# Performance work log

Measured on AMD Instinct MI355X. Metric: run time of the kernel, lower is better.

The kernel has to match this reference:

```python
import jax, jax.numpy as jnp
import numpy as np


def _grid_sample_3d(src, grid):
    """Trilinear grid_sample, align_corners=True, zero padding.
    src: [B,C,D,H,W], grid: [B,D,H,W,3] with last dim (x,y,z) ~ (W,H,D) in [-1,1].
    """
    B, C, D, H, W = src.shape
    gx, gy, gz = grid[..., 0], grid[..., 1], grid[..., 2]
    # unnormalize (align_corners=True): -1 -> 0, +1 -> dim-1
    ix = (gx + 1.0) * ((W - 1) / 2.0)
    iy = (gy + 1.0) * ((H - 1) / 2.0)
    iz = (gz + 1.0) * ((D - 1) / 2.0)
    ix0 = jnp.floor(ix); iy0 = jnp.floor(iy); iz0 = jnp.floor(iz)
    fx = ix - ix0; fy = iy - iy0; fz = iz - iz0  # fractional parts
    x0 = ix0.astype(jnp.int32); y0 = iy0.astype(jnp.int32); z0 = iz0.astype(jnp.int32)

    src_flat = src.reshape(B, C, D * H * W)
    out = jnp.zeros((B, C, D * H * W), dtype=src.dtype)
    for dz in (0, 1):
        for dy in (0, 1):
            for dx in (0, 1):
                xc = x0 + dx; yc = y0 + dy; zc = z0 + dz
                w = ((fx if dx else 1.0 - fx)
                     * (fy if dy else 1.0 - fy)
                     * (fz if dz else 1.0 - fz))
                valid = ((xc >= 0) & (xc < W) & (yc >= 0) & (yc < H)
                         & (zc >= 0) & (zc < D))
                xs = jnp.clip(xc, 0, W - 1)
                ys = jnp.clip(yc, 0, H - 1)
                zs = jnp.clip(zc, 0, D - 1)
                lin = ((zs * H + ys) * W + xs).reshape(B, -1)  # [B, DHW]
                vals = jax.vmap(lambda s, i: jnp.take(s, i, axis=1))(src_flat, lin)  # [B,C,DHW]
                out = out + (w * valid).reshape(B, 1, -1).astype(src.dtype) * vals
    return out.reshape(B, C, D, H, W)


def _affine_grid_3d(theta, D, H, W):
    """torch affine_grid (align_corners=True) for size [B,3,D,H,W]. Returns [B,D,H,W,3]."""
    xs = jnp.linspace(-1.0, 1.0, W, dtype=theta.dtype)
    ys = jnp.linspace(-1.0, 1.0, H, dtype=theta.dtype)
    zs = jnp.linspace(-1.0, 1.0, D, dtype=theta.dtype)
    bx = jnp.broadcast_to(xs[None, None, :], (D, H, W))
    by = jnp.broadcast_to(ys[None, :, None], (D, H, W))
    bz = jnp.broadcast_to(zs[:, None, None], (D, H, W))
    base = jnp.stack([bx, by, bz, jnp.ones((D, H, W), theta.dtype)], axis=-1)  # [D,H,W,4]
    return jnp.einsum('bij,dhwj->bdhwi', theta, base)


def setup_inputs() -> dict:
    key = jax.random.key(0)
    k1, k2 = jax.random.split(key)
    B, C, D, H, W = 2, 2, 160, 192, 224
    src = jax.random.normal(k1, (B, C, D, H, W), dtype=jnp.float32)
    eye = jnp.concatenate([jnp.eye(3, dtype=jnp.float32),
                           jnp.zeros((3, 1), jnp.float32)], axis=1)  # [3,4]
    mat = eye[None] + 0.05 * jax.random.normal(k2, (B, 3, 4), dtype=jnp.float32)
    return {"src": src, "mat": mat}


def reference(src, mat):
    B, C, D, H, W = src.shape
    norm = jnp.array([[1, 1, 1, D], [1, 1, 1, H], [1, 1, 1, W]], dtype=mat.dtype)
    theta = mat / norm[None]  # normalize translation column by spatial dims
    grid = _affine_grid_3d(theta, D, H, W)
    return _grid_sample_3d(src, grid)
```

## Files before the change

kernel.cpp:

```cpp
#include <hip/hip_runtime.h>

#define BB 2
#define CC 2
#define DD 160
#define HH 192
#define WW 224
#define DHW (DD * HH * WW)

typedef float f2v __attribute__((ext_vector_type(2)));

__device__ __forceinline__ f2v load2u(const float* p) {
    struct __attribute__((packed)) S { f2v v; };
    return ((const S*)p)->v;
}

__global__ __launch_bounds__(256) void affine_sample_kernel(
    const float* __restrict__ src,
    const float* __restrict__ mat,
    float* __restrict__ out)
{
    int idx = blockIdx.x * blockDim.x + threadIdx.x;
    if (idx >= DHW) return;
    int b = blockIdx.y;

    int w = idx % WW;
    int t = idx / WW;
    int h = t % HH;
    int d = t / HH;

    const float* m = mat + b * 12;
    float a00 = m[0], a01 = m[1], a02 = m[2],  a03 = m[3]  * (1.0f / (float)DD);
    float a10 = m[4], a11 = m[5], a12 = m[6],  a13 = m[7]  * (1.0f / (float)HH);
    float a20 = m[8], a21 = m[9], a22 = m[10], a23 = m[11] * (1.0f / (float)WW);

    float xn = -1.0f + (float)w * (2.0f / (float)(WW - 1));
    float yn = -1.0f + (float)h * (2.0f / (float)(HH - 1));
    float zn = -1.0f + (float)d * (2.0f / (float)(DD - 1));

    float gx = a00 * xn + a01 * yn + a02 * zn + a03;
    float gy = a10 * xn + a11 * yn + a12 * zn + a13;
    float gz = a20 * xn + a21 * yn + a22 * zn + a23;

    float ix = (gx + 1.0f) * ((float)(WW - 1) * 0.5f);
    float iy = (gy + 1.0f) * ((float)(HH - 1) * 0.5f);
    float iz = (gz + 1.0f) * ((float)(DD - 1) * 0.5f);

    float fx0 = floorf(ix), fy0 = floorf(iy), fz0 = floorf(iz);
    float fx = ix - fx0, fy = iy - fy0, fz = iz - fz0;
    int x0 = (int)fx0, y0 = (int)fy0, z0 = (int)fz0;
    int x1 = x0 + 1, y1 = y0 + 1, z1 = z0 + 1;

    float wx0 = (x0 >= 0 && x0 < WW) ? (1.0f - fx) : 0.0f;
    float wx1 = (x1 >= 0 && x1 < WW) ? fx          : 0.0f;
    float wy0 = (y0 >= 0 && y0 < HH) ? (1.0f - fy) : 0.0f;
    float wy1 = (y1 >= 0 && y1 < HH) ? fy          : 0.0f;
    float wz0 = (z0 >= 0 && z0 < DD) ? (1.0f - fz) : 0.0f;
    float wz1 = (z1 >= 0 && z1 < DD) ? fz          : 0.0f;

    int xc0 = min(max(x0, 0), WW - 1), xc1 = min(max(x1, 0), WW - 1);
    int yc0 = min(max(y0, 0), HH - 1), yc1 = min(max(y1, 0), HH - 1);
    int zc0 = min(max(z0, 0), DD - 1), zc1 = min(max(z1, 0), DD - 1);

    int xb   = min(xc0, WW - 2);
    int sel0 = xc0 - xb;
    int sel1 = xc1 - xb;

    const float* s0 = src + (size_t)b * CC * DHW + xb;
    const float* s1 = s0 + DHW;

    int r00 = (zc0 * HH + yc0) * WW;
    int r01 = (zc0 * HH + yc1) * WW;
    int r10 = (zc1 * HH + yc0) * WW;
    int r11 = (zc1 * HH + yc1) * WW;

    f2v pa00 = load2u(s0 + r00);
    f2v pa01 = load2u(s0 + r01);
    f2v pa10 = load2u(s0 + r10);
    f2v pa11 = load2u(s0 + r11);
    f2v pb00 = load2u(s1 + r00);
    f2v pb01 = load2u(s1 + r01);
    f2v pb10 = load2u(s1 + r10);
    f2v pb11 = load2u(s1 + r11);

    float w00 = wz0 * wy0, w01 = wz0 * wy1;
    float w10 = wz1 * wy0, w11 = wz1 * wy1;

    #define ROWVAL(p) (wx0 * (sel0 ? (p)[1] : (p)[0]) + wx1 * (sel1 ? (p)[1] : (p)[0]))
    float acc0 = w00 * ROWVAL(pa00) + w01 * ROWVAL(pa01)
               + w10 * ROWVAL(pa10) + w11 * ROWVAL(pa11);
    float acc1 = w00 * ROWVAL(pb00) + w01 * ROWVAL(pb01)
               + w10 * ROWVAL(pb10) + w11 * ROWVAL(pb11);
    #undef ROWVAL

    float* o = out + (size_t)b * CC * DHW + idx;
    __builtin_nontemporal_store(acc0, o);
    __builtin_nontemporal_store(acc1, o + DHW);
}

extern "C" void kernel_launch(void* const* d_in, const int* in_sizes, int n_in,
                              void* d_out, int out_size, void* d_ws, size_t ws_size,
                              hipStream_t stream) {
    const float* src = (const float*)d_in[0];
    const float* mat = (const float*)d_in[1];
    float* out = (float*)d_out;

    dim3 block(256);
    dim3 grid((DHW + 255) / 256, BB);
    affine_sample_kernel<<<grid, block, 0, stream>>>(src, mat, out);
}
```

Baseline: 250.6 us.

## Process four voxels per thread with vector stores and XCD-aware block swizzle

Each thread now computes four consecutive output voxels along W. The grid coordinate is stepped incrementally, all 32 two-float gathers are issued before the math, and results go out as 128-bit nontemporal stores. Block indices are remapped so that each of the 8 XCDs gets a contiguous chunk of the volume, to improve L2 locality of the gathered source. The x-selection is folded into per-voxel weights to cut per-sample selects. The cost is higher register pressure and fewer blocks. The code also relies on W being divisible by 4 and DHW dividing evenly by the block work size.

```diff
diff --git a/kernel.cpp b/kernel.cpp
--- a/kernel.cpp
+++ b/kernel.cpp
@@ -7,24 +7,32 @@
 #define WW 224
 #define DHW (DD * HH * WW)
 
+#define VPT 4
+#define TPB 256
+#define NBX (DHW / (TPB * VPT))
+#define NXCD 8
+#define CPX (NBX / NXCD)
+
 typedef float f2v __attribute__((ext_vector_type(2)));
+typedef float f4v __attribute__((ext_vector_type(4)));
 
 __device__ __forceinline__ f2v load2u(const float* p) {
     struct __attribute__((packed)) S { f2v v; };
     return ((const S*)p)->v;
 }
 
-__global__ __launch_bounds__(256) void affine_sample_kernel(
+__global__ __launch_bounds__(TPB) void affine_sample_kernel(
     const float* __restrict__ src,
     const float* __restrict__ mat,
     float* __restrict__ out)
 {
-    int idx = blockIdx.x * blockDim.x + threadIdx.x;
-    if (idx >= DHW) return;
+    int bx  = blockIdx.x;
+    int sbx = (bx & (NXCD - 1)) * CPX + (bx >> 3);
+    int base = (sbx * TPB + (int)threadIdx.x) * VPT;
     int b = blockIdx.y;
 
-    int w = idx % WW;
-    int t = idx / WW;
+    int w = base % WW;
+    int t = base / WW;
     int h = t % HH;
     int d = t / HH;
 
@@ -37,64 +45,89 @@
     float yn = -1.0f + (float)h * (2.0f / (float)(HH - 1));
     float zn = -1.0f + (float)d * (2.0f / (float)(DD - 1));
 
-    float gx = a00 * xn + a01 * yn + a02 * zn + a03;
-    float gy = a10 * xn + a11 * yn + a12 * zn + a13;
-    float gz = a20 * xn + a21 * yn + a22 * zn + a23;
+    float ix = (a00 * xn + a01 * yn + a02 * zn + a03 + 1.0f) * ((float)(WW - 1) * 0.5f);
+    float iy = (a10 * xn + a11 * yn + a12 * zn + a13 + 1.0f) * ((float)(HH - 1) * 0.5f);
+    float iz = (a20 * xn + a21 * yn + a22 * zn + a23 + 1.0f) * ((float)(DD - 1) * 0.5f);
 
-    float ix = (gx + 1.0f) * ((float)(WW - 1) * 0.5f);
-    float iy = (gy + 1.0f) * ((float)(HH - 1) * 0.5f);
-    float iz = (gz + 1.0f) * ((float)(DD - 1) * 0.5f);
+    float dix = a00;
+    float diy = a10 * ((float)(HH - 1) / (float)(WW - 1));
+    float diz = a20 * ((float)(DD - 1) / (float)(WW - 1));
 
-    float fx0 = floorf(ix), fy0 = floorf(iy), fz0 = floorf(iz);
-    float fx = ix - fx0, fy = iy - fy0, fz = iz - fz0;
-    int x0 = (int)fx0, y0 = (int)fy0, z0 = (int)fz0;
-    int x1 = x0 + 1, y1 = y0 + 1, z1 = z0 + 1;
+    const float* sb = src + (size_t)b * (CC * DHW);
 
-    float wx0 = (x0 >= 0 && x0 < WW) ? (1.0f - fx) : 0.0f;
-    float wx1 = (x1 >= 0 && x1 < WW) ? fx          : 0.0f;
-    float wy0 = (y0 >= 0 && y0 < HH) ? (1.0f - fy) : 0.0f;
-    float wy1 = (y1 >= 0 && y1 < HH) ? fy          : 0.0f;
-    float wz0 = (z0 >= 0 && z0 < DD) ? (1.0f - fz) : 0.0f;
-    float wz1 = (z1 >= 0 && z1 < DD) ? fz          : 0.0f;
+    f2v   P0[VPT][4], P1[VPT][4];
+    float q0a[VPT], q1a[VPT];
+    float wzy0[VPT], wzy1[VPT], wzy2[VPT], wzy3[VPT];
 
-    int xc0 = min(max(x0, 0), WW - 1), xc1 = min(max(x1, 0), WW - 1);
-    int yc0 = min(max(y0, 0), HH - 1), yc1 = min(max(y1, 0), HH - 1);
-    int zc0 = min(max(z0, 0), DD - 1), zc1 = min(max(z1, 0), DD - 1);
+    #pragma unroll
+    for (int v = 0; v < VPT; ++v) {
+        float ixv = fmaf((float)v, dix, ix);
+        float iyv = fmaf((float)v, diy, iy);
+        float izv = fmaf((float)v, diz, iz);
 
-    int xb   = min(xc0, WW - 2);
-    int sel0 = xc0 - xb;
-    int sel1 = xc1 - xb;
+        float fx0 = floorf(ixv), fy0 = floorf(iyv), fz0 = floorf(izv);
+        float fx = ixv - fx0, fy = iyv - fy0, fz = izv - fz0;
+        int x0 = (int)fx0, y0 = (int)fy0, z0 = (int)fz0;
+        int x1 = x0 + 1, y1 = y0 + 1, z1 = z0 + 1;
 
-    const float* s0 = src + (size_t)b * CC * DHW + xb;
-    const float* s1 = s0 + DHW;
+        float wx0 = (x0 >= 0 && x0 < WW) ? (1.0f - fx) : 0.0f;
+        float wx1 = (x1 >= 0 && x1 < WW) ? fx          : 0.0f;
+        float wy0 = (y0 >= 0 && y0 < HH) ? (1.0f - fy) : 0.0f;
+        float wy1 = (y1 >= 0 && y1 < HH) ? fy          : 0.0f;
+        float wz0 = (z0 >= 0 && z0 < DD) ? (1.0f - fz) : 0.0f;
+        float wz1 = (z1 >= 0 && z1 < DD) ? fz          : 0.0f;
 
-    int r00 = (zc0 * HH + yc0) * WW;
-    int r01 = (zc0 * HH + yc1) * WW;
-    int r10 = (zc1 * HH + yc0) * WW;
-    int r11 = (zc1 * HH + yc1) * WW;
+        int xc0 = min(max(x0, 0), WW - 1), xc1 = min(max(x1, 0), WW - 1);
+        int yc0 = min(max(y0, 0), HH - 1), yc1 = min(max(y1, 0), HH - 1);
+        int zc0 = min(max(z0, 0), DD - 1), zc1 = min(max(z1, 0), DD - 1);
 
-    f2v pa00 = load2u(s0 + r00);
-    f2v pa01 = load2u(s0 + r01);
-    f2v pa10 = load2u(s0 + r10);
-    f2v pa11 = load2u(s0 + r11);
-    f2v pb00 = load2u(s1 + r00);
-    f2v pb01 = load2u(s1 + r01);
-    f2v pb10 = load2u(s1 + r10);
-    f2v pb11 = load2u(s1 + r11);
+        int xb   = min(xc0, WW - 2);
+        int sel0 = xc0 - xb;
+        int sel1 = xc1 - xb;
 
-    float w00 = wz0 * wy0, w01 = wz0 * wy1;
-    float w10 = wz1 * wy0, w11 = wz1 * wy1;
+        q0a[v] = (sel0 ? 0.0f : wx0) + (sel1 ? 0.0f : wx1);
+        q1a[v] = (sel0 ? wx0 : 0.0f) + (sel1 ? wx1 : 0.0f);
 
-    #define ROWVAL(p) (wx0 * (sel0 ? (p)[1] : (p)[0]) + wx1 * (sel1 ? (p)[1] : (p)[0]))
-    float acc0 = w00 * ROWVAL(pa00) + w01 * ROWVAL(pa01)
-               + w10 * ROWVAL(pa10) + w11 * ROWVAL(pa11);
-    float acc1 = w00 * ROWVAL(pb00) + w01 * ROWVAL(pb01)
-               + w10 * ROWVAL(pb10) + w11 * ROWVAL(pb11);
-    #undef ROWVAL
+        wzy0[v] = wz0 * wy0; wzy1[v] = wz0 * wy1;
+        wzy2[v] = wz1 * wy0; wzy3[v] = wz1 * wy1;
 
-    float* o = out + (size_t)b * CC * DHW + idx;
-    __builtin_nontemporal_store(acc0, o);
-    __builtin_nontemporal_store(acc1, o + DHW);
+        int zh0 = zc0 * HH, zh1 = zc1 * HH;
+        int r0 = (zh0 + yc0) * WW + xb;
+        int r1 = (zh0 + yc1) * WW + xb;
+        int r2 = (zh1 + yc0) * WW + xb;
+        int r3 = (zh1 + yc1) * WW + xb;
+
+        P0[v][0] = load2u(sb + r0);
+        P0[v][1] = load2u(sb + r1);
+        P0[v][2] = load2u(sb + r2);
+        P0[v][3] = load2u(sb + r3);
+        P1[v][0] = load2u(sb + (DHW + r0));
+        P1[v][1] = load2u(sb + (DHW + r1));
+        P1[v][2] = load2u(sb + (DHW + r2));
+        P1[v][3] = load2u(sb + (DHW + r3));
+    }
+
+    f4v o0, o1;
+    #pragma unroll
+    for (int v = 0; v < VPT; ++v) {
+        float rq00 = wzy0[v] * q0a[v], rq01 = wzy0[v] * q1a[v];
+        float rq10 = wzy1[v] * q0a[v], rq11 = wzy1[v] * q1a[v];
+        float rq20 = wzy2[v] * q0a[v], rq21 = wzy2[v] * q1a[v];
+        float rq30 = wzy3[v] * q0a[v], rq31 = wzy3[v] * q1a[v];
+
+        o0[v] = rq00 * P0[v][0][0] + rq01 * P0[v][0][1]
+              + rq10 * P0[v][1][0] + rq11 * P0[v][1][1]
+              + rq20 * P0[v][2][0] + rq21 * P0[v][2][1]
+              + rq30 * P0[v][3][0] + rq31 * P0[v][3][1];
+        o1[v] = rq00 * P1[v][0][0] + rq01 * P1[v][0][1]
+              + rq10 * P1[v][1][0] + rq11 * P1[v][1][1]
+              + rq20 * P1[v][2][0] + rq21 * P1[v][2][1]
+              + rq30 * P1[v][3][0] + rq31 * P1[v][3][1];
+    }
+
+    float* ob = out + (size_t)b * (CC * DHW) + base;
+    __builtin_nontemporal_store(o0, (f4v*)ob);
+    __builtin_nontemporal_store(o1, (f4v*)(ob + DHW));
 }
 
 extern "C" void kernel_launch(void* const* d_in, const int* in_sizes, int n_in,
@@ -104,7 +137,7 @@
     const float* mat = (const float*)d_in[1];
     float* out = (float*)d_out;
 
-    dim3 block(256);
-    dim3 grid((DHW + 255) / 256, BB);
+    dim3 block(TPB);
+    dim3 grid(NBX, BB);
     affine_sample_kernel<<<grid, block, 0, stream>>>(src, mat, out);
 }
```

Result: slower. 281.1 us (+12.2%).

## Compute two adjacent outputs per thread sharing 4-wide row loads

Applied to the files above, without the earlier changes.

Each thread now produces two x-adjacent output voxels. When both fall in the same y/z cells it serves them from shared 16-byte row loads (dwordx4 via inline asm), and it falls back to separate loads when the cells differ. The change also remaps block IDs so each XCD gets a contiguous range of the volume, sets launch bounds to 4 blocks per unit, and writes 8-byte stores. The aim is fewer load instructions and better L2 locality, at the cost of more registers, a divergent fallback path and a forced full vmcnt wait.

```diff
diff --git a/kernel.cpp b/kernel.cpp
--- a/kernel.cpp
+++ b/kernel.cpp
@@ -7,24 +7,42 @@
 #define WW 224
 #define DHW (DD * HH * WW)
 
+#define TPB 256
+#define NBX (DHW / (TPB * 2))
+#define NXCD 8
+#define CPX (NBX / NXCD)
+
 typedef float f2v __attribute__((ext_vector_type(2)));
+typedef float f4v __attribute__((ext_vector_type(4)));
+
+__device__ __forceinline__ f4v qload(const float* __restrict__ base, int byteoff) {
+    f4v r;
+    asm volatile("global_load_dwordx4 %0, %1, %2"
+                 : "=v"(r) : "v"(byteoff), "s"(base));
+    return r;
+}
 
 __device__ __forceinline__ f2v load2u(const float* p) {
     struct __attribute__((packed)) S { f2v v; };
     return ((const S*)p)->v;
 }
 
-__global__ __launch_bounds__(256) void affine_sample_kernel(
+__device__ __forceinline__ f2v vlo(f4v q) { return __builtin_shufflevector(q, q, 0, 1); }
+__device__ __forceinline__ f2v vhi(f4v q) { return __builtin_shufflevector(q, q, 2, 3); }
+
+__global__ __launch_bounds__(TPB, 4) void affine_sample_kernel(
     const float* __restrict__ src,
     const float* __restrict__ mat,
     float* __restrict__ out)
 {
-    int idx = blockIdx.x * blockDim.x + threadIdx.x;
-    if (idx >= DHW) return;
+    int bx  = blockIdx.x;
+    int sbx = (bx & (NXCD - 1)) * CPX + (bx >> 3);
+    int pid  = sbx * TPB + (int)threadIdx.x;
+    int base = pid * 2;
     int b = blockIdx.y;
 
-    int w = idx % WW;
-    int t = idx / WW;
+    int w = base % WW;
+    int t = base / WW;
     int h = t % HH;
     int d = t / HH;
 
@@ -37,64 +55,114 @@
     float yn = -1.0f + (float)h * (2.0f / (float)(HH - 1));
     float zn = -1.0f + (float)d * (2.0f / (float)(DD - 1));
 
-    float gx = a00 * xn + a01 * yn + a02 * zn + a03;
-    float gy = a10 * xn + a11 * yn + a12 * zn + a13;
-    float gz = a20 * xn + a21 * yn + a22 * zn + a23;
+    float ixA = (a00*xn + a01*yn + a02*zn + a03 + 1.0f) * ((float)(WW-1)*0.5f);
+    float iyA = (a10*xn + a11*yn + a12*zn + a13 + 1.0f) * ((float)(HH-1)*0.5f);
+    float izA = (a20*xn + a21*yn + a22*zn + a23 + 1.0f) * ((float)(DD-1)*0.5f);
+    float ixB = ixA + a00;
+    float iyB = iyA + a10 * ((float)(HH-1)/(float)(WW-1));
+    float izB = izA + a20 * ((float)(DD-1)/(float)(WW-1));
 
-    float ix = (gx + 1.0f) * ((float)(WW - 1) * 0.5f);
-    float iy = (gy + 1.0f) * ((float)(HH - 1) * 0.5f);
-    float iz = (gz + 1.0f) * ((float)(DD - 1) * 0.5f);
+    float fy0A = floorf(iyA), fz0A = floorf(izA);
+    float fyA = iyA - fy0A,   fzA = izA - fz0A;
+    int y0A = (int)fy0A, z0A = (int)fz0A;
+    float wy0A = (y0A >= 0   && y0A < HH)     ? 1.0f - fyA : 0.0f;
+    float wy1A = (y0A >= -1  && y0A < HH - 1) ? fyA        : 0.0f;
+    float wz0A = (z0A >= 0   && z0A < DD)     ? 1.0f - fzA : 0.0f;
+    float wz1A = (z0A >= -1  && z0A < DD - 1) ? fzA        : 0.0f;
+    int yc0A = min(max(y0A, 0), HH - 1), yc1A = min(max(y0A + 1, 0), HH - 1);
+    int zc0A = min(max(z0A, 0), DD - 1), zc1A = min(max(z0A + 1, 0), DD - 1);
 
-    float fx0 = floorf(ix), fy0 = floorf(iy), fz0 = floorf(iz);
-    float fx = ix - fx0, fy = iy - fy0, fz = iz - fz0;
-    int x0 = (int)fx0, y0 = (int)fy0, z0 = (int)fz0;
-    int x1 = x0 + 1, y1 = y0 + 1, z1 = z0 + 1;
+    float fy0B = floorf(iyB), fz0B = floorf(izB);
+    float fyB = iyB - fy0B,   fzB = izB - fz0B;
+    int y0B = (int)fy0B, z0B = (int)fz0B;
+    float wy0B = (y0B >= 0   && y0B < HH)     ? 1.0f - fyB : 0.0f;
+    float wy1B = (y0B >= -1  && y0B < HH - 1) ? fyB        : 0.0f;
+    float wz0B = (z0B >= 0   && z0B < DD)     ? 1.0f - fzB : 0.0f;
+    float wz1B = (z0B >= -1  && z0B < DD - 1) ? fzB        : 0.0f;
+    int yc0B = min(max(y0B, 0), HH - 1), yc1B = min(max(y0B + 1, 0), HH - 1);
+    int zc0B = min(max(z0B, 0), DD - 1), zc1B = min(max(z0B + 1, 0), DD - 1);
 
-    float wx0 = (x0 >= 0 && x0 < WW) ? (1.0f - fx) : 0.0f;
-    float wx1 = (x1 >= 0 && x1 < WW) ? fx          : 0.0f;
-    float wy0 = (y0 >= 0 && y0 < HH) ? (1.0f - fy) : 0.0f;
-    float wy1 = (y1 >= 0 && y1 < HH) ? fy          : 0.0f;
-    float wz0 = (z0 >= 0 && z0 < DD) ? (1.0f - fz) : 0.0f;
-    float wz1 = (z1 >= 0 && z1 < DD) ? fz          : 0.0f;
+    int x0A = (int)floorf(ixA);
+    int x0B = (int)floorf(ixB);
+    int xbJ = min(max(x0A, 0), WW - 4);
+    float bxj = (float)xbJ;
+    float hA0 = fmaxf(0.0f, 1.0f - fabsf(ixA - bxj));
+    float hA1 = fmaxf(0.0f, 1.0f - fabsf(ixA - (bxj + 1.0f)));
+    float hA2 = fmaxf(0.0f, 1.0f - fabsf(ixA - (bxj + 2.0f)));
+    float hA3 = fmaxf(0.0f, 1.0f - fabsf(ixA - (bxj + 3.0f)));
+    float hB0 = fmaxf(0.0f, 1.0f - fabsf(ixB - bxj));
+    float hB1 = fmaxf(0.0f, 1.0f - fabsf(ixB - (bxj + 1.0f)));
+    float hB2 = fmaxf(0.0f, 1.0f - fabsf(ixB - (bxj + 2.0f)));
+    float hB3 = fmaxf(0.0f, 1.0f - fabsf(ixB - (bxj + 3.0f)));
 
-    int xc0 = min(max(x0, 0), WW - 1), xc1 = min(max(x1, 0), WW - 1);
-    int yc0 = min(max(y0, 0), HH - 1), yc1 = min(max(y1, 0), HH - 1);
-    int zc0 = min(max(z0, 0), DD - 1), zc1 = min(max(z1, 0), DD - 1);
-
-    int xb   = min(xc0, WW - 2);
-    int sel0 = xc0 - xb;
-    int sel1 = xc1 - xb;
-
-    const float* s0 = src + (size_t)b * CC * DHW + xb;
+    const float* s0 = src + (size_t)b * (CC * DHW);
     const float* s1 = s0 + DHW;
 
-    int r00 = (zc0 * HH + yc0) * WW;
-    int r01 = (zc0 * HH + yc1) * WW;
-    int r10 = (zc1 * HH + yc0) * WW;
-    int r11 = (zc1 * HH + yc1) * WW;
+    int r0 = ((zc0A * HH + yc0A) * WW + xbJ) * 4;
+    int r1 = ((zc0A * HH + yc1A) * WW + xbJ) * 4;
+    int r2 = ((zc1A * HH + yc0A) * WW + xbJ) * 4;
+    int r3 = ((zc1A * HH + yc1A) * WW + xbJ) * 4;
 
-    f2v pa00 = load2u(s0 + r00);
-    f2v pa01 = load2u(s0 + r01);
-    f2v pa10 = load2u(s0 + r10);
-    f2v pa11 = load2u(s0 + r11);
-    f2v pb00 = load2u(s1 + r00);
-    f2v pb01 = load2u(s1 + r01);
-    f2v pb10 = load2u(s1 + r10);
-    f2v pb11 = load2u(s1 + r11);
+    f4v qa0 = qload(s0, r0), qa1 = qload(s0, r1), qa2 = qload(s0, r2), qa3 = qload(s0, r3);
+    f4v qb0 = qload(s1, r0), qb1 = qload(s1, r1), qb2 = qload(s1, r2), qb3 = qload(s1, r3);
 
-    float w00 = wz0 * wy0, w01 = wz0 * wy1;
-    float w10 = wz1 * wy0, w11 = wz1 * wy1;
+    float rwA0 = wz0A * wy0A, rwA1 = wz0A * wy1A, rwA2 = wz1A * wy0A, rwA3 = wz1A * wy1A;
+    float rwB0 = wz0B * wy0B, rwB1 = wz0B * wy1B, rwB2 = wz1B * wy0B, rwB3 = wz1B * wy1B;
 
-    #define ROWVAL(p) (wx0 * (sel0 ? (p)[1] : (p)[0]) + wx1 * (sel1 ? (p)[1] : (p)[0]))
-    float acc0 = w00 * ROWVAL(pa00) + w01 * ROWVAL(pa01)
-               + w10 * ROWVAL(pa10) + w11 * ROWVAL(pa11);
-    float acc1 = w00 * ROWVAL(pb00) + w01 * ROWVAL(pb01)
-               + w10 * ROWVAL(pb10) + w11 * ROWVAL(pb11);
-    #undef ROWVAL
+    bool neq = (yc0B != yc0A) | (yc1B != yc1A) | (zc0B != zc0A) | (zc1B != zc1A);
+    float fb0 = 0.0f, fb1 = 0.0f;
+    if (neq) {
+        int xbB = min(max(x0B, 0), WW - 2);
+        float u0 = fmaxf(0.0f, 1.0f - fabsf(ixB - (float)xbB));
+        float u1 = fmaxf(0.0f, 1.0f - fabsf(ixB - (float)(xbB + 1)));
+        int e0 = (zc0B * HH + yc0B) * WW + xbB;
+        int e1 = (zc0B * HH + yc1B) * WW + xbB;
+        int e2 = (zc1B * HH + yc0B) * WW + xbB;
+        int e3 = (zc1B * HH + yc1B) * WW + xbB;
+        f2v p0 = load2u(s0 + e0), p1 = load2u(s0 + e1), p2 = load2u(s0 + e2), p3 = load2u(s0 + e3);
+        f2v g0 = load2u(s1 + e0), g1 = load2u(s1 + e1), g2 = load2u(s1 + e2), g3 = load2u(s1 + e3);
+        fb0 = rwB0 * (u0 * p0.x + u1 * p0.y) + rwB1 * (u0 * p1.x + u1 * p1.y)
+            + rwB2 * (u0 * p2.x + u1 * p2.y) + rwB3 * (u0 * p3.x + u1 * p3.y);
+        fb1 = rwB0 * (u0 * g0.x + u1 * g0.y) + rwB1 * (u0 * g1.x + u1 * g1.y)
+            + rwB2 * (u0 * g2.x + u1 * g2.y) + rwB3 * (u0 * g3.x + u1 * g3.y);
+    }
 
-    float* o = out + (size_t)b * CC * DHW + idx;
-    __builtin_nontemporal_store(acc0, o);
-    __builtin_nontemporal_store(acc1, o + DHW);
+    asm volatile("s_waitcnt vmcnt(0)" ::: "memory");
+    __builtin_amdgcn_sched_barrier(0);
+
+    f2v hA01; hA01.x = hA0; hA01.y = hA1;
+    f2v hA23; hA23.x = hA2; hA23.y = hA3;
+    f2v hB01; hB01.x = hB0; hB01.y = hB1;
+    f2v hB23; hB23.x = hB2; hB23.y = hB3;
+
+    f2v mA0a = rwA0 * hA01, mA0b = rwA0 * hA23;
+    f2v mA1a = rwA1 * hA01, mA1b = rwA1 * hA23;
+    f2v mA2a = rwA2 * hA01, mA2b = rwA2 * hA23;
+    f2v mA3a = rwA3 * hA01, mA3b = rwA3 * hA23;
+    f2v mB0a = rwB0 * hB01, mB0b = rwB0 * hB23;
+    f2v mB1a = rwB1 * hB01, mB1b = rwB1 * hB23;
+    f2v mB2a = rwB2 * hB01, mB2b = rwB2 * hB23;
+    f2v mB3a = rwB3 * hB01, mB3b = rwB3 * hB23;
+
+    f2v vA0 = mA0a * vlo(qa0) + mA0b * vhi(qa0) + mA1a * vlo(qa1) + mA1b * vhi(qa1)
+            + mA2a * vlo(qa2) + mA2b * vhi(qa2) + mA3a * vlo(qa3) + mA3b * vhi(qa3);
+    f2v vA1 = mA0a * vlo(qb0) + mA0b * vhi(qb0) + mA1a * vlo(qb1) + mA1b * vhi(qb1)
+            + mA2a * vlo(qb2) + mA2b * vhi(qb2) + mA3a * vlo(qb3) + mA3b * vhi(qb3);
+    f2v vB0 = mB0a * vlo(qa0) + mB0b * vhi(qa0) + mB1a * vlo(qa1) + mB1b * vhi(qa1)
+            + mB2a * vlo(qa2) + mB2b * vhi(qa2) + mB3a * vlo(qa3) + mB3b * vhi(qa3);
+    f2v vB1 = mB0a * vlo(qb0) + mB0b * vhi(qb0) + mB1a * vlo(qb1) + mB1b * vhi(qb1)
+            + mB2a * vlo(qb2) + mB2b * vhi(qb2) + mB3a * vlo(qb3) + mB3b * vhi(qb3);
+
+    float accA0 = vA0.x + vA0.y;
+    float accA1 = vA1.x + vA1.y;
+    float accB0 = neq ? fb0 : (vB0.x + vB0.y);
+    float accB1 = neq ? fb1 : (vB1.x + vB1.y);
+
+    float* o = out + (size_t)b * (CC * DHW) + base;
+    f2v st0; st0.x = accA0; st0.y = accB0;
+    f2v st1; st1.x = accA1; st1.y = accB1;
+    __builtin_nontemporal_store(st0, (f2v*)o);
+    __builtin_nontemporal_store(st1, (f2v*)(o + DHW));
 }
 
 extern "C" void kernel_launch(void* const* d_in, const int* in_sizes, int n_in,
@@ -104,7 +172,7 @@
     const float* mat = (const float*)d_in[1];
     float* out = (float*)d_out;
 
-    dim3 block(256);
-    dim3 grid((DHW + 255) / 256, BB);
+    dim3 block(TPB);
+    dim3 grid(NBX, BB);
     affine_sample_kernel<<<grid, block, 0, stream>>>(src, mat, out);
 }
```

Result: slower. 260.1 us (+3.8%).
